# Kernel tuning notes

Measured on AMD Instinct MI355X. Metric: run time of the kernel, lower is better.

## Reference

```python
import jax, jax.numpy as jnp
import numpy as np

N_EMBD = 1024
HEAD_SIZE = 64
BATCH = 4
T = 4096  # == block_size


def setup_inputs() -> dict:
    key = jax.random.key(0)
    kx, kq, kk, kv = jax.random.split(key, 4)
    x = jax.random.normal(kx, (BATCH, T, N_EMBD), dtype=jnp.float32)
    Wq = jax.random.normal(kq, (N_EMBD, HEAD_SIZE), dtype=jnp.float32) * 0.02
    Wk = jax.random.normal(kk, (N_EMBD, HEAD_SIZE), dtype=jnp.float32) * 0.02
    Wv = jax.random.normal(kv, (N_EMBD, HEAD_SIZE), dtype=jnp.float32) * 0.02
    return {"x": x, "Wq": Wq, "Wk": Wk, "Wv": Wv}


def reference(x, Wq, Wk, Wv):
    # x: [B, T, C]; projections: [B, T, H]
    B, Tlen, C = x.shape
    q = jnp.einsum('btc,ch->bth', x, Wq)
    k = jnp.einsum('btc,ch->bth', x, Wk)
    v = jnp.einsum('btc,ch->bth', x, Wv)
    # NOTE: original scales by C**-0.5 where C = n_embd (input channels), not head_size
    scale = jnp.asarray(C, x.dtype) ** -0.5
    wei = jnp.einsum('bth,bsh->bts', q, k) * scale  # [B, T, T]
    causal = jnp.tril(jnp.ones((Tlen, Tlen), dtype=bool))
    wei = jnp.where(causal, wei, -jnp.inf)
    wei = jax.nn.softmax(wei, axis=-1)
    # dropout p=0.0 -> identity
    out = jnp.einsum('bts,bsh->bth', wei, v)  # [B, T, H]
    return out
```

## Files before the change

### kernel.cpp

```cpp
#include <hip/hip_runtime.h>
#include <math.h>

#define T_SEQ 4096
#define NBATCH 4
#define NEMBD 1024
#define HS 64
#define BT (NBATCH * T_SEQ)

typedef float f32x4 __attribute__((ext_vector_type(4)));
typedef short s8v  __attribute__((ext_vector_type(8)));
typedef short s4v  __attribute__((ext_vector_type(4)));

__device__ __forceinline__ short f2b_rne(float f) {
    union { float f; unsigned u; } v; v.f = f;
    unsigned r = v.u + 0x7fffu + ((v.u >> 16) & 1u);
    return (short)(r >> 16);
}
__device__ __forceinline__ unsigned pk2(float lo, float hi) {
    return __builtin_amdgcn_perm(__float_as_uint(hi), __float_as_uint(lo), 0x07060302u);
}

__global__ __launch_bounds__(256) void wtrans_kernel(
        const float* __restrict__ Wq, const float* __restrict__ Wk,
        const float* __restrict__ Wv, short* __restrict__ Wt) {
    int e = blockIdx.x * 256 + threadIdx.x;
    int col = e & 63, k = (e >> 6) & 1023, mat = e >> 16;
    const float* W = (mat == 0) ? Wq : ((mat == 1) ? Wk : Wv);
    float scale = (mat == 0) ? 0.0450842298f : 1.0f;
    Wt[(size_t)(mat * 64 + col) * 1024 + k] = f2b_rne(W[k * 64 + col] * scale);
}

__global__ __launch_bounds__(512, 4) void proj_kernel(
        const float* __restrict__ x, const short* __restrict__ Wt,
        short* __restrict__ QKV) {
    __shared__ short xs[32 * 72];
    int tid = threadIdx.x;
    int w = tid >> 6, l = tid & 63, quad = l >> 4, c16 = l & 15;
    int rt = w >> 2, ws = w & 3;
    int row0 = blockIdx.x * 32;
    short* VpT = QKV + 2 * (size_t)BT * HS;

    int srow = tid >> 4, skc = (tid & 15) * 4;
    const float* gx = x + (size_t)(row0 + srow) * NEMBD + skc;
    const short* wp = Wt + (size_t)(ws * 48 + c16) * 1024;

    float4 pf = *(const float4*)gx;
    f32x4 acc[3] = {};

    for (int ko = 0; ko < NEMBD; ko += 64) {
        {
            union { s4v v; unsigned u[2]; } pkv;
            pkv.u[0] = pk2(pf.x, pf.y); pkv.u[1] = pk2(pf.z, pf.w);
            *(s4v*)(xs + srow * 72 + skc) = pkv.v;
        }
        __syncthreads();
        {
            int kn = (ko + 64 < NEMBD) ? (ko + 64) : 0;
            pf = *(const float4*)(gx + kn);
        }
        #pragma unroll
        for (int ks = 0; ks < 2; ks++) {
            s8v a = *(const s8v*)(xs + (rt * 16 + c16) * 72 + ks * 32 + quad * 8);
            #pragma unroll
            for (int j = 0; j < 3; j++) {
                s8v b = *(const s8v*)(wp + (size_t)j * 16 * 1024 + ko + ks * 32 + quad * 8);
                acc[j] = __builtin_amdgcn_mfma_f32_16x16x32_bf16(a, b, acc[j], 0, 0, 0);
            }
        }
        __syncthreads();
    }
    #pragma unroll
    for (int j = 0; j < 3; j++) {
        int g = ws * 48 + j * 16 + c16;
        int mat = g >> 6, h = g & 63;
        if (mat < 2) {
            #pragma unroll
            for (int r = 0; r < 4; r++) {
                int row = row0 + rt * 16 + quad * 4 + r;
                QKV[(size_t)mat * BT * HS + (size_t)row * HS + h] = f2b_rne(acc[j][r]);
            }
        } else {
            s4v pv;
            #pragma unroll
            for (int r = 0; r < 4; r++) pv[r] = f2b_rne(acc[j][r]);
            *(s4v*)(VpT + (size_t)h * BT + row0 + rt * 16 + quad * 4) = pv;
        }
    }
}

__global__ __launch_bounds__(512, 4) void attn_kernel(
        const short* __restrict__ QKV, float* __restrict__ out) {
    __shared__ float smem[9216];
    short* Ps = (short*)smem;

    int tid = threadIdx.x;
    int w = tid >> 6, l = tid & 63, quad = l >> 4, c16 = l & 15;
    int bi = blockIdx.x;
    int b  = bi & 3;
    int jt = 127 - (bi >> 2);
    int q0 = jt * 32;

    const short* Qp  = QKV;
    const short* Kp  = QKV + (size_t)BT * HS;
    const short* VpT = QKV + 2 * (size_t)BT * HS;
    size_t bT = (size_t)b * T_SEQ;

    s8v qf[2][2];
    #pragma unroll
    for (int qt = 0; qt < 2; qt++)
        #pragma unroll
        for (int h = 0; h < 2; h++)
            qf[qt][h] = *(const s8v*)(Qp + (bT + q0 + qt * 16 + c16) * HS + h * 32 + quad * 8);

    f32x4 o[2][4] = {};
    float lsum[2] = {0.f, 0.f};
    int nkt = (q0 >> 6) + 1;
    short* Pw[2] = { Ps + (w * 2) * 1152, Ps + (w * 2 + 1) * 1152 };

    for (int kt = w; kt < nkt; kt += 8) {
        int kb = kt * 64;
        bool last = (kt == nkt - 1);
        f32x4 st[2][4];
        #pragma unroll
        for (int nt = 0; nt < 4; nt++) {
            const short* kr = Kp + (bT + kb + nt * 16 + c16) * HS + quad * 8;
            s8v k0 = *(const s8v*)kr;
            s8v k1 = *(const s8v*)(kr + 32);
            f32x4 z0 = {0.f, 0.f, 0.f, 0.f}, z1 = {0.f, 0.f, 0.f, 0.f};
            z0 = __builtin_amdgcn_mfma_f32_16x16x32_bf16(k0, qf[0][0], z0, 0, 0, 0);
            z0 = __builtin_amdgcn_mfma_f32_16x16x32_bf16(k1, qf[0][1], z0, 0, 0, 0);
            z1 = __builtin_amdgcn_mfma_f32_16x16x32_bf16(k0, qf[1][0], z1, 0, 0, 0);
            z1 = __builtin_amdgcn_mfma_f32_16x16x32_bf16(k1, qf[1][1], z1, 0, 0, 0);
            st[0][nt] = z0; st[1][nt] = z1;
        }
        #pragma unroll
        for (int qt = 0; qt < 2; qt++) {
            int qrow = q0 + qt * 16 + c16;
            #pragma unroll
            for (int nt = 0; nt < 4; nt++) {
                float p[4];
                #pragma unroll
                for (int r = 0; r < 4; r++) {
                    float v = st[qt][nt][r];
                    if (last && (kb + nt * 16 + quad * 4 + r > qrow)) v = -30000.f;
                    p[r] = __builtin_amdgcn_exp2f(v);
                    lsum[qt] += p[r];
                }
                union { s4v v; unsigned u[2]; } pkv;
                pkv.u[0] = pk2(p[0], p[1]); pkv.u[1] = pk2(p[2], p[3]);
                *(s4v*)(Pw[qt] + c16 * 72 + nt * 16 + quad * 4) = pkv.v;
            }
        }
        s8v pa[2][2];
        #pragma unroll
        for (int qt = 0; qt < 2; qt++) {
            pa[qt][0] = *(const s8v*)(Pw[qt] + c16 * 72 + quad * 8);
            pa[qt][1] = *(const s8v*)(Pw[qt] + c16 * 72 + quad * 8 + 32);
        }
        #pragma unroll
        for (int nt = 0; nt < 4; nt++) {
            const short* vr = VpT + (size_t)(nt * 16 + c16) * BT + bT + kb + quad * 8;
            s8v v0 = *(const s8v*)vr;
            s8v v1 = *(const s8v*)(vr + 32);
            #pragma unroll
            for (int qt = 0; qt < 2; qt++) {
                o[qt][nt] = __builtin_amdgcn_mfma_f32_16x16x32_bf16(pa[qt][0], v0, o[qt][nt], 0, 0, 0);
                o[qt][nt] = __builtin_amdgcn_mfma_f32_16x16x32_bf16(pa[qt][1], v1, o[qt][nt], 0, 0, 0);
            }
        }
    }

    #pragma unroll
    for (int qt = 0; qt < 2; qt++) {
        lsum[qt] += __shfl_xor(lsum[qt], 16);
        lsum[qt] += __shfl_xor(lsum[qt], 32);
    }

    #pragma unroll
    for (int qt = 0; qt < 2; qt++) {
        __syncthreads();
        #pragma unroll
        for (int nt = 0; nt < 4; nt++)
            *(f32x4*)(smem + ((w * 4 + nt) * 64 + l) * 4) = o[qt][nt];
        if (l < 16) smem[8192 + w * 16 + l] = lsum[qt];
        __syncthreads();
        if (w < 4) {
            f32x4 os = {0.f, 0.f, 0.f, 0.f}, ls = {0.f, 0.f, 0.f, 0.f};
            #pragma unroll
            for (int s = 0; s < 8; s++) {
                os += *(const f32x4*)(smem + ((s * 4 + w) * 64 + l) * 4);
                ls += *(const f32x4*)(smem + 8192 + s * 16 + quad * 4);
            }
            #pragma unroll
            for (int r = 0; r < 4; r++)
                out[(bT + q0 + qt * 16 + quad * 4 + r) * HS + w * 16 + c16] = os[r] / ls[r];
        }
    }
}

extern "C" void kernel_launch(void* const* d_in, const int* in_sizes, int n_in,
                              void* d_out, int out_size, void* d_ws, size_t ws_size,
                              hipStream_t stream) {
    const float* x  = (const float*)d_in[0];
    const float* Wq = (const float*)d_in[1];
    const float* Wk = (const float*)d_in[2];
    const float* Wv = (const float*)d_in[3];
    float* out = (float*)d_out;

    short* QKV = (short*)d_ws;
    short* Wt  = QKV + (size_t)3 * BT * HS;

    wtrans_kernel<<<768, 256, 0, stream>>>(Wq, Wk, Wv, Wt);
    proj_kernel<<<BT / 32, 512, 0, stream>>>(x, Wt, QKV);
    attn_kernel<<<512, 512, 0, stream>>>(QKV, out);
}
```

Measured before the change: 185.5 us.

## Stage projection weights in LDS, pre-cast x to bf16, tile V layout

The projection kernel now stages the full 192x64 weight slice in shared memory for each k-step instead of reading it per-wave from global memory. When the workspace is large enough, x is first cast to bf16 in a separate kernel so the projection reads half the bytes. Otherwise a touch kernel pre-reads x, apparently to warm the cache. V^T is also stored in 64x64 tiles per key block so the attention kernel's V loads are contiguous. These changes add extra kernel launches and a full extra pass over x, and they raise LDS use, which may lower occupancy.

```diff
diff --git a/kernel.cpp b/kernel.cpp
--- a/kernel.cpp
+++ b/kernel.cpp
@@ -18,6 +18,34 @@
 }
 __device__ __forceinline__ unsigned pk2(float lo, float hi) {
     return __builtin_amdgcn_perm(__float_as_uint(hi), __float_as_uint(lo), 0x07060302u);
+}
+
+__global__ __launch_bounds__(256) void xcast_kernel(
+        const float* __restrict__ x, short* __restrict__ xb) {
+    size_t i = ((size_t)blockIdx.x * 256 + threadIdx.x) * 16;
+    float4 a = *(const float4*)(x + i);
+    float4 b = *(const float4*)(x + i + 4);
+    float4 c = *(const float4*)(x + i + 8);
+    float4 d = *(const float4*)(x + i + 12);
+    union { s8v v; unsigned u[4]; } v0, v1;
+    v0.u[0] = pk2(a.x, a.y); v0.u[1] = pk2(a.z, a.w);
+    v0.u[2] = pk2(b.x, b.y); v0.u[3] = pk2(b.z, b.w);
+    v1.u[0] = pk2(c.x, c.y); v1.u[1] = pk2(c.z, c.w);
+    v1.u[2] = pk2(d.x, d.y); v1.u[3] = pk2(d.z, d.w);
+    *(s8v*)(xb + i) = v0.v;
+    *(s8v*)(xb + i + 8) = v1.v;
+}
+
+__global__ __launch_bounds__(256) void xtouch_kernel(
+        const float* __restrict__ x, float* __restrict__ sink) {
+    const float4* p = (const float4*)x;
+    float s = 0.f;
+    #pragma unroll
+    for (int it = 0; it < 8; it++) {
+        float4 v = p[(size_t)blockIdx.x * 2048 + it * 256 + threadIdx.x];
+        s += v.x + v.y + v.z + v.w;
+    }
+    if (s == 1.0e38f) sink[0] = s;
 }
 
 __global__ __launch_bounds__(256) void wtrans_kernel(
@@ -30,40 +58,73 @@
     Wt[(size_t)(mat * 64 + col) * 1024 + k] = f2b_rne(W[k * 64 + col] * scale);
 }
 
-__global__ __launch_bounds__(512, 4) void proj_kernel(
-        const float* __restrict__ x, const short* __restrict__ Wt,
+template<bool SRC_BF16>
+__global__ __launch_bounds__(512) void proj_kernel(
+        const void* __restrict__ xsrc, const short* __restrict__ Wt,
         short* __restrict__ QKV) {
     __shared__ short xs[32 * 72];
+    __shared__ short wsh[192 * 72];
     int tid = threadIdx.x;
     int w = tid >> 6, l = tid & 63, quad = l >> 4, c16 = l & 15;
-    int rt = w >> 2, ws = w & 3;
+    int rt = w >> 2, cg = w & 3;
     int row0 = blockIdx.x * 32;
     short* VpT = QKV + 2 * (size_t)BT * HS;
 
-    int srow = tid >> 4, skc = (tid & 15) * 4;
-    const float* gx = x + (size_t)(row0 + srow) * NEMBD + skc;
-    const short* wp = Wt + (size_t)(ws * 48 + c16) * 1024;
-
-    float4 pf = *(const float4*)gx;
+    const short* xb = (const short*)xsrc;
+    const float* xf = (const float*)xsrc;
+    int xrow_b = tid >> 3,  xc8 = (tid & 7) * 8;
+    int xrow_f = tid >> 4,  xc4 = (tid & 15) * 4;
+    int wrow = 0;
+
+    s8v  wreg[3];
+    s8v  xreg_b;
+    float4 xreg_f;
+    #pragma unroll
+    for (int i = 0; i < 3; i++) {
+        int c = tid + 512 * i;
+        wreg[i] = *(const s8v*)(Wt + (size_t)(c >> 3) * 1024 + ((c & 7) * 8));
+    }
+    if (SRC_BF16) {
+        if (tid < 256) xreg_b = *(const s8v*)(xb + (size_t)(row0 + xrow_b) * 1024 + xc8);
+    } else {
+        xreg_f = *(const float4*)(xf + (size_t)(row0 + xrow_f) * 1024 + xc4);
+    }
+
     f32x4 acc[3] = {};
-
     for (int ko = 0; ko < NEMBD; ko += 64) {
-        {
+        #pragma unroll
+        for (int i = 0; i < 3; i++) {
+            int c = tid + 512 * i;
+            *(s8v*)(wsh + (c >> 3) * 72 + ((c & 7) * 8)) = wreg[i];
+        }
+        if (SRC_BF16) {
+            if (tid < 256) *(s8v*)(xs + xrow_b * 72 + xc8) = xreg_b;
+        } else {
             union { s4v v; unsigned u[2]; } pkv;
-            pkv.u[0] = pk2(pf.x, pf.y); pkv.u[1] = pk2(pf.z, pf.w);
-            *(s4v*)(xs + srow * 72 + skc) = pkv.v;
+            pkv.u[0] = pk2(xreg_f.x, xreg_f.y);
+            pkv.u[1] = pk2(xreg_f.z, xreg_f.w);
+            *(s4v*)(xs + xrow_f * 72 + xc4) = pkv.v;
         }
         __syncthreads();
         {
             int kn = (ko + 64 < NEMBD) ? (ko + 64) : 0;
-            pf = *(const float4*)(gx + kn);
+            #pragma unroll
+            for (int i = 0; i < 3; i++) {
+                int c = tid + 512 * i;
+                wreg[i] = *(const s8v*)(Wt + (size_t)(c >> 3) * 1024 + kn + ((c & 7) * 8));
+            }
+            if (SRC_BF16) {
+                if (tid < 256) xreg_b = *(const s8v*)(xb + (size_t)(row0 + xrow_b) * 1024 + kn + xc8);
+            } else {
+                xreg_f = *(const float4*)(xf + (size_t)(row0 + xrow_f) * 1024 + kn + xc4);
+            }
         }
         #pragma unroll
         for (int ks = 0; ks < 2; ks++) {
             s8v a = *(const s8v*)(xs + (rt * 16 + c16) * 72 + ks * 32 + quad * 8);
             #pragma unroll
             for (int j = 0; j < 3; j++) {
-                s8v b = *(const s8v*)(wp + (size_t)j * 16 * 1024 + ko + ks * 32 + quad * 8);
+                s8v b = *(const s8v*)(wsh + (cg * 48 + j * 16 + c16) * 72 + ks * 32 + quad * 8);
                 acc[j] = __builtin_amdgcn_mfma_f32_16x16x32_bf16(a, b, acc[j], 0, 0, 0);
             }
         }
@@ -71,7 +132,7 @@
     }
     #pragma unroll
     for (int j = 0; j < 3; j++) {
-        int g = ws * 48 + j * 16 + c16;
+        int g = cg * 48 + j * 16 + c16;
         int mat = g >> 6, h = g & 63;
         if (mat < 2) {
             #pragma unroll
@@ -80,10 +141,13 @@
                 QKV[(size_t)mat * BT * HS + (size_t)row * HS + h] = f2b_rne(acc[j][r]);
             }
         } else {
+            int tg = row0 + rt * 16 + quad * 4;
+            int b = tg >> 12, t = tg & 4095;
+            size_t base = (((size_t)((b * 64 + (t >> 6)) * 64 + h)) << 6) + (t & 63);
             s4v pv;
             #pragma unroll
             for (int r = 0; r < 4; r++) pv[r] = f2b_rne(acc[j][r]);
-            *(s4v*)(VpT + (size_t)h * BT + row0 + rt * 16 + quad * 4) = pv;
+            *(s4v*)(VpT + base) = pv;
         }
     }
 }
@@ -159,7 +223,7 @@
         }
         #pragma unroll
         for (int nt = 0; nt < 4; nt++) {
-            const short* vr = VpT + (size_t)(nt * 16 + c16) * BT + bT + kb + quad * 8;
+            const short* vr = VpT + (((size_t)((b * 64 + kt) * 64 + nt * 16 + c16)) << 6) + quad * 8;
             s8v v0 = *(const s8v*)vr;
             s8v v1 = *(const s8v*)(vr + 32);
             #pragma unroll
@@ -209,8 +273,16 @@
 
     short* QKV = (short*)d_ws;
     short* Wt  = QKV + (size_t)3 * BT * HS;
+    short* xb  = Wt + (size_t)192 * 1024;
+    size_t need = ((size_t)3 * BT * HS + (size_t)192 * 1024 + (size_t)BT * NEMBD) * 2;
 
     wtrans_kernel<<<768, 256, 0, stream>>>(Wq, Wk, Wv, Wt);
-    proj_kernel<<<BT / 32, 512, 0, stream>>>(x, Wt, QKV);
+    if (ws_size >= need) {
+        xcast_kernel<<<4096, 256, 0, stream>>>(x, xb);
+        proj_kernel<true><<<BT / 32, 512, 0, stream>>>(xb, Wt, QKV);
+    } else {
+        xtouch_kernel<<<2048, 256, 0, stream>>>(x, (float*)d_ws);
+        proj_kernel<false><<<BT / 32, 512, 0, stream>>>(x, Wt, QKV);
+    }
     attn_kernel<<<512, 512, 0, stream>>>(QKV, out);
 }
```

After: 175.6 us. 5.3% less time.
